# Performance work log

Hardware: AMD Instinct MI355X
Metric: run time of the kernel (lower is better)

Reference implementation:

```python
import jax, jax.numpy as jnp
import numpy as np

N = 100000       # num_nodes
E = 1600000      # num_edges (avg degree 16)
EL = 200000      # link-prediction edges
IN_C = 64
POS = 16
HID = 64
OUT = 32


def setup_inputs() -> dict:
    key = jax.random.key(0)
    ks = jax.random.split(key, 10)
    def glorot(k, shape):
        scale = 1.0 / np.sqrt(shape[0])
        return jax.random.uniform(k, shape, jnp.float32, -scale, scale)
    return {
        "x": jax.random.normal(ks[0], (N, IN_C), jnp.float32),
        "pos_emb": jax.random.normal(ks[1], (N, POS), jnp.float32),
        "W1": glorot(ks[2], (IN_C + POS, HID)),
        "b1": jnp.zeros((HID,), jnp.float32),
        "W2": glorot(ks[3], (HID, OUT)),
        "b2": jnp.zeros((OUT,), jnp.float32),
        "Wl": glorot(ks[4], (2 * OUT, 1)),
        "bl": jnp.zeros((1,), jnp.float32),
        "edge_index": jax.random.randint(ks[5], (2, E), 0, N, jnp.int32),
        "edge_label_index": jax.random.randint(ks[6], (2, EL), 0, N, jnp.int32),
    }


def reference(x, pos_emb, W1, b1, W2, b2, Wl, bl, edge_index, edge_label_index):
    n = x.shape[0]
    # GCNConv: add self-loops, symmetric deg^{-1/2} normalization (PyG defaults)
    loops = jnp.arange(n, dtype=edge_index.dtype)
    src = jnp.concatenate([edge_index[0], loops])  # [E+N]
    dst = jnp.concatenate([edge_index[1], loops])  # [E+N]
    deg = jax.ops.segment_sum(jnp.ones_like(dst, jnp.float32), dst, num_segments=n)
    dinv = jnp.where(deg > 0, jax.lax.rsqrt(jnp.maximum(deg, 1e-12)), 0.0)
    norm = dinv[src] * dinv[dst]  # [E+N]

    def gcn_conv(h, W, b):
        hw = h @ W                                    # [N, d_out] transform first
        msg = hw[src] * norm[:, None]                 # gather + normalize
        return jax.ops.segment_sum(msg, dst, num_segments=n) + b  # scatter-add

    h = jnp.concatenate([x, pos_emb], axis=1)         # [N, in+pos]
    h = jax.nn.relu(gcn_conv(h, W1, b1))              # dropout is eval no-op
    z = gcn_conv(h, W2, b2)                           # [N, out]

    s, d = edge_label_index[0], edge_label_index[1]
    zc = jnp.concatenate([z[s], z[d]], axis=1)        # [EL, 2*out]
    edge_pred = (zc @ Wl + bl)[:, 0]                  # [EL]
    return z, edge_pred
```

## Files before the change

kernel.cpp:

```cpp
#include <hip/hip_runtime.h>
#include <hip/hip_fp16.h>

#define NN 100000
#define NE 1600000
#define NEL 200000

#define NBUCK 196
#define CAPB  10240
#define TPE   8192

typedef short s16x8 __attribute__((ext_vector_type(8)));
typedef float f32x4 __attribute__((ext_vector_type(4)));

__device__ __forceinline__ unsigned short bf16hi(float v) {
    unsigned u = __float_as_uint(v);
    return (unsigned short)((u + 0x7FFFu + ((u >> 16) & 1u)) >> 16);
}
__device__ __forceinline__ float bf16tof(unsigned short b) {
    return __uint_as_float(((unsigned)b) << 16);
}

__global__ __launch_bounds__(256) void k_part(const int* __restrict__ src,
                                              const int* __restrict__ dst,
                                              int* __restrict__ gcur,
                                              int* __restrict__ part) {
    __shared__ int hist[NBUCK];
    __shared__ int base[NBUCK];
    __shared__ int rk[NBUCK];
    int tid = threadIdx.x;
    for (int i = tid; i < NBUCK; i += 256) { hist[i] = 0; rk[i] = 0; }
    __syncthreads();
    int e0 = blockIdx.x * TPE;
    int e1 = min(e0 + TPE, NE);
    for (int e = e0 + tid; e < e1; e += 256)
        atomicAdd(&hist[dst[e] >> 9], 1);
    __syncthreads();
    for (int i = tid; i < NBUCK; i += 256)
        base[i] = i * CAPB + atomicAdd(&gcur[i], hist[i]);
    __syncthreads();
    for (int e = e0 + tid; e < e1; e += 256) {
        int d = dst[e];
        int s = src[e];
        int b = d >> 9;
        int r = atomicAdd(&rk[b], 1);
        part[base[b] + r] = ((d & 511) << 17) | s;
    }
}

__global__ __launch_bounds__(256) void k_build(const int* __restrict__ gcur,
                                               const int* __restrict__ part,
                                               int* __restrict__ csr,
                                               int* __restrict__ off,
                                               float* __restrict__ dinv) {
    __shared__ int cnts[256];
    __shared__ int hist[512];
    __shared__ int loff[512];
    __shared__ int ssum[256];
    __shared__ int csrbuf[CAPB];
    int b = blockIdx.x;
    int tid = threadIdx.x;
    cnts[tid] = (tid < NBUCK) ? gcur[tid] : 0;
    __syncthreads();
    for (int st = 1; st < 256; st <<= 1) {
        int tmp = (tid >= st) ? cnts[tid - st] : 0;
        __syncthreads();
        cnts[tid] += tmp;
        __syncthreads();
    }
    int obase = (b == 0) ? 0 : cnts[b - 1];
    int cnt = gcur[b];
    int pbase = b * CAPB;
    hist[tid] = 0; hist[tid + 256] = 0;
    __syncthreads();
    for (int i = tid; i < cnt; i += 256)
        atomicAdd(&hist[part[pbase + i] >> 17], 1);
    __syncthreads();
    int a0 = hist[2 * tid], a1 = hist[2 * tid + 1];
    int pairs = a0 + a1;
    ssum[tid] = pairs;
    __syncthreads();
    for (int st = 1; st < 256; st <<= 1) {
        int tmp = (tid >= st) ? ssum[tid - st] : 0;
        __syncthreads();
        ssum[tid] += tmp;
        __syncthreads();
    }
    int pexcl = ssum[tid] - pairs;
    loff[2 * tid] = pexcl;
    loff[2 * tid + 1] = pexcl + a0;
    __syncthreads();
    for (int i = tid; i < 512; i += 256) {
        int d = b * 512 + i;
        if (d < NN) {
            int c = hist[i];
            off[d] = obase + loff[i] + c;
            dinv[d] = rsqrtf((float)(c + 1));
        }
    }
    hist[tid] = 0; hist[tid + 256] = 0;
    __syncthreads();
    for (int i = tid; i < cnt; i += 256) {
        int rec = part[pbase + i];
        int dl = rec >> 17;
        int r = atomicAdd(&hist[dl], 1);
        csrbuf[loff[dl] + r] = rec & 0x1FFFF;
    }
    __syncthreads();
    for (int i = tid; i < cnt; i += 256)
        csr[obase + i] = csrbuf[i];
}

#define HW1_K 104
__global__ __launch_bounds__(256) void k_hw1(const float* __restrict__ x,
                                             const float* __restrict__ pos,
                                             const float* __restrict__ W1,
                                             const float* __restrict__ dinv,
                                             __half* __restrict__ hw1) {
    __shared__ unsigned short ahi[64 * HW1_K];
    __shared__ unsigned short alo[64 * HW1_K];
    __shared__ unsigned short bhi[64 * HW1_K];
    __shared__ unsigned short blo[64 * HW1_K];
    __shared__ float sdin[64];
    int tid = threadIdx.x;
    int nb = blockIdx.x * 64;
    for (int i = tid; i < 64 * 24; i += 256) {
        int r = i / 24, c = i - r * 24;
        ahi[r * HW1_K + 80 + c] = 0; alo[r * HW1_K + 80 + c] = 0;
        bhi[r * HW1_K + 80 + c] = 0; blo[r * HW1_K + 80 + c] = 0;
    }
    for (int i = tid; i < 64 * 64; i += 256) {
        int r = i >> 6, c = i & 63;
        int g = nb + r;
        float v = (g < NN) ? x[g * 64 + c] : 0.0f;
        unsigned short h = bf16hi(v);
        ahi[r * HW1_K + c] = h;
        alo[r * HW1_K + c] = bf16hi(v - bf16tof(h));
    }
    for (int i = tid; i < 64 * 16; i += 256) {
        int r = i >> 4, c = i & 15;
        int g = nb + r;
        float v = (g < NN) ? pos[g * 16 + c] : 0.0f;
        unsigned short h = bf16hi(v);
        ahi[r * HW1_K + 64 + c] = h;
        alo[r * HW1_K + 64 + c] = bf16hi(v - bf16tof(h));
    }
    for (int i = tid; i < 80 * 64; i += 256) {
        int k = i >> 6, c = i & 63;
        float v = W1[i];
        unsigned short h = bf16hi(v);
        bhi[c * HW1_K + k] = h;
        blo[c * HW1_K + k] = bf16hi(v - bf16tof(h));
    }
    for (int i = tid; i < 64; i += 256) {
        int g = nb + i;
        sdin[i] = (g < NN) ? dinv[g] : 0.0f;
    }
    __syncthreads();
    int wave = tid >> 6, lane = tid & 63;
    int frow = lane & 15, fq = lane >> 4;
    int r0 = wave * 16;
    int aoff = (r0 + frow) * HW1_K + fq * 8;
    s16x8 ah0 = *(s16x8*)&ahi[aoff];
    s16x8 ah1 = *(s16x8*)&ahi[aoff + 32];
    s16x8 ah2 = *(s16x8*)&ahi[aoff + 64];
    s16x8 al0 = *(s16x8*)&alo[aoff];
    s16x8 al1 = *(s16x8*)&alo[aoff + 32];
    s16x8 al2 = *(s16x8*)&alo[aoff + 64];
    f32x4 acc[4];
#pragma unroll
    for (int ct = 0; ct < 4; ++ct) {
        acc[ct] = (f32x4)(0.0f);
        int boff = (ct * 16 + frow) * HW1_K + fq * 8;
        s16x8 bh0 = *(s16x8*)&bhi[boff];
        s16x8 bh1 = *(s16x8*)&bhi[boff + 32];
        s16x8 bh2 = *(s16x8*)&bhi[boff + 64];
        s16x8 bl0 = *(s16x8*)&blo[boff];
        s16x8 bl1 = *(s16x8*)&blo[boff + 32];
        s16x8 bl2 = *(s16x8*)&blo[boff + 64];
        acc[ct] = __builtin_amdgcn_mfma_f32_16x16x32_bf16(ah0, bh0, acc[ct], 0, 0, 0);
        acc[ct] = __builtin_amdgcn_mfma_f32_16x16x32_bf16(ah1, bh1, acc[ct], 0, 0, 0);
        acc[ct] = __builtin_amdgcn_mfma_f32_16x16x32_bf16(ah2, bh2, acc[ct], 0, 0, 0);
        acc[ct] = __builtin_amdgcn_mfma_f32_16x16x32_bf16(ah0, bl0, acc[ct], 0, 0, 0);
        acc[ct] = __builtin_amdgcn_mfma_f32_16x16x32_bf16(ah1, bl1, acc[ct], 0, 0, 0);
        acc[ct] = __builtin_amdgcn_mfma_f32_16x16x32_bf16(ah2, bl2, acc[ct], 0, 0, 0);
        acc[ct] = __builtin_amdgcn_mfma_f32_16x16x32_bf16(al0, bh0, acc[ct], 0, 0, 0);
        acc[ct] = __builtin_amdgcn_mfma_f32_16x16x32_bf16(al1, bh1, acc[ct], 0, 0, 0);
        acc[ct] = __builtin_amdgcn_mfma_f32_16x16x32_bf16(al2, bh2, acc[ct], 0, 0, 0);
    }
#pragma unroll
    for (int ct = 0; ct < 4; ++ct) {
        int col = ct * 16 + frow;
#pragma unroll
        for (int i = 0; i < 4; ++i) {
            int r = r0 + fq * 4 + i;
            int g = nb + r;
            if (g < NN)
                hw1[g * 64 + col] = __float2half_rn(acc[ct][i] * sdin[r]);
        }
    }
}

__global__ __launch_bounds__(256) void k_gather1(const int* __restrict__ off,
                                                 const int* __restrict__ csr,
                                                 const float* __restrict__ dinv,
                                                 const __half* __restrict__ hw,
                                                 const float* __restrict__ b1,
                                                 __half* __restrict__ h2out) {
    int lane = threadIdx.x & 63;
    int wave = threadIdx.x >> 6;
    int d = blockIdx.x * 4 + wave;
    int start = (d == 0) ? 0 : off[d - 1];
    int end = off[d];
    start = __builtin_amdgcn_readfirstlane(start);
    end   = __builtin_amdgcn_readfirstlane(end);
    float dd = dinv[d];
    float hself = __half2float(hw[d * 64 + lane]);
    float acc0 = 0.0f, acc1 = 0.0f, acc2 = 0.0f, acc3 = 0.0f;
    for (int e = start; e < end; e += 16) {
        int rem = end - e;
        int s0 = csr[e];
        int s1  = (rem > 1)  ? csr[e + 1]  : s0;
        int s2  = (rem > 2)  ? csr[e + 2]  : s0;
        int s3  = (rem > 3)  ? csr[e + 3]  : s0;
        int s4  = (rem > 4)  ? csr[e + 4]  : s0;
        int s5  = (rem > 5)  ? csr[e + 5]  : s0;
        int s6  = (rem > 6)  ? csr[e + 6]  : s0;
        int s7  = (rem > 7)  ? csr[e + 7]  : s0;
        int s8  = (rem > 8)  ? csr[e + 8]  : s0;
        int s9  = (rem > 9)  ? csr[e + 9]  : s0;
        int s10 = (rem > 10) ? csr[e + 10] : s0;
        int s11 = (rem > 11) ? csr[e + 11] : s0;
        int s12 = (rem > 12) ? csr[e + 12] : s0;
        int s13 = (rem > 13) ? csr[e + 13] : s0;
        int s14 = (rem > 14) ? csr[e + 14] : s0;
        int s15 = (rem > 15) ? csr[e + 15] : s0;
        float g0  = __half2float(hw[s0  * 64 + lane]);
        float g1  = __half2float(hw[s1  * 64 + lane]);
        float g2  = __half2float(hw[s2  * 64 + lane]);
        float g3  = __half2float(hw[s3  * 64 + lane]);
        float g4  = __half2float(hw[s4  * 64 + lane]);
        float g5  = __half2float(hw[s5  * 64 + lane]);
        float g6  = __half2float(hw[s6  * 64 + lane]);
        float g7  = __half2float(hw[s7  * 64 + lane]);
        float g8  = __half2float(hw[s8  * 64 + lane]);
        float g9  = __half2float(hw[s9  * 64 + lane]);
        float g10 = __half2float(hw[s10 * 64 + lane]);
        float g11 = __half2float(hw[s11 * 64 + lane]);
        float g12 = __half2float(hw[s12 * 64 + lane]);
        float g13 = __half2float(hw[s13 * 64 + lane]);
        float g14 = __half2float(hw[s14 * 64 + lane]);
        float g15 = __half2float(hw[s15 * 64 + lane]);
        int inv = 16 - rem;
        if (inv < 0) inv = 0;
        acc0 += g0;  acc1 += g1;  acc2 += g2;  acc3 += g3;
        acc0 += g4;  acc1 += g5;  acc2 += g6;  acc3 += g7;
        acc0 += g8;  acc1 += g9;  acc2 += g10; acc3 += g11;
        acc0 += g12; acc1 += g13; acc2 += g14; acc3 += g15;
        acc3 = fmaf(-(float)inv, g0, acc3);
    }
    float v = fmaxf(b1[lane] + dd * (((acc0 + acc1) + (acc2 + acc3)) + hself), 0.0f);
    h2out[d * 64 + lane] = __float2half_rn(v);
}

#define HW2_K 72
__global__ __launch_bounds__(256) void k_hw2(const __half* __restrict__ h2,
                                             const float* __restrict__ W2,
                                             const float* __restrict__ dinv,
                                             __half* __restrict__ hw2) {
    __shared__ unsigned short ahi[128 * HW2_K];
    __shared__ unsigned short alo[128 * HW2_K];
    __shared__ unsigned short bhi[32 * HW2_K];
    __shared__ unsigned short blo[32 * HW2_K];
    __shared__ float sdin[128];
    int tid = threadIdx.x;
    int nb = blockIdx.x * 128;
    for (int i = tid; i < 128 * 32; i += 256) {
        int r = i >> 5, cp = i & 31;
        int g = nb + r;
        __half2 hv = (g < NN) ? ((const __half2*)h2)[g * 32 + cp]
                              : __floats2half2_rn(0.0f, 0.0f);
        float2 f = __half22float2(hv);
        unsigned short h0 = bf16hi(f.x), h1 = bf16hi(f.y);
        ahi[r * HW2_K + 2 * cp]     = h0;
        ahi[r * HW2_K + 2 * cp + 1] = h1;
        alo[r * HW2_K + 2 * cp]     = bf16hi(f.x - bf16tof(h0));
        alo[r * HW2_K + 2 * cp + 1] = bf16hi(f.y - bf16tof(h1));
    }
    for (int i = tid; i < 64 * 32; i += 256) {
        int k = i >> 5, c = i & 31;
        float v = W2[i];
        unsigned short h = bf16hi(v);
        bhi[c * HW2_K + k] = h;
        blo[c * HW2_K + k] = bf16hi(v - bf16tof(h));
    }
    for (int i = tid; i < 128; i += 256) {
        int g = nb + i;
        sdin[i] = (g < NN) ? dinv[g] : 0.0f;
    }
    __syncthreads();
    int wave = tid >> 6, lane = tid & 63;
    int frow = lane & 15, fq = lane >> 4;
    int r0 = wave * 32;
    f32x4 acc[2][2];
#pragma unroll
    for (int rt = 0; rt < 2; ++rt) {
        int aoff = (r0 + rt * 16 + frow) * HW2_K + fq * 8;
        s16x8 ah0 = *(s16x8*)&ahi[aoff];
        s16x8 ah1 = *(s16x8*)&ahi[aoff + 32];
        s16x8 al0 = *(s16x8*)&alo[aoff];
        s16x8 al1 = *(s16x8*)&alo[aoff + 32];
#pragma unroll
        for (int ct = 0; ct < 2; ++ct) {
            acc[rt][ct] = (f32x4)(0.0f);
            int boff = (ct * 16 + frow) * HW2_K + fq * 8;
            s16x8 bh0 = *(s16x8*)&bhi[boff];
            s16x8 bh1 = *(s16x8*)&bhi[boff + 32];
            s16x8 bl0 = *(s16x8*)&blo[boff];
            s16x8 bl1 = *(s16x8*)&blo[boff + 32];
            acc[rt][ct] = __builtin_amdgcn_mfma_f32_16x16x32_bf16(ah0, bh0, acc[rt][ct], 0, 0, 0);
            acc[rt][ct] = __builtin_amdgcn_mfma_f32_16x16x32_bf16(ah1, bh1, acc[rt][ct], 0, 0, 0);
            acc[rt][ct] = __builtin_amdgcn_mfma_f32_16x16x32_bf16(ah0, bl0, acc[rt][ct], 0, 0, 0);
            acc[rt][ct] = __builtin_amdgcn_mfma_f32_16x16x32_bf16(ah1, bl1, acc[rt][ct], 0, 0, 0);
            acc[rt][ct] = __builtin_amdgcn_mfma_f32_16x16x32_bf16(al0, bh0, acc[rt][ct], 0, 0, 0);
            acc[rt][ct] = __builtin_amdgcn_mfma_f32_16x16x32_bf16(al1, bh1, acc[rt][ct], 0, 0, 0);
        }
    }
#pragma unroll
    for (int rt = 0; rt < 2; ++rt)
#pragma unroll
        for (int ct = 0; ct < 2; ++ct) {
            int col = ct * 16 + frow;
#pragma unroll
            for (int i = 0; i < 4; ++i) {
                int r = r0 + rt * 16 + fq * 4 + i;
                int g = nb + r;
                if (g < NN)
                    hw2[g * 32 + col] = __float2half_rn(acc[rt][ct][i] * sdin[r]);
            }
        }
}

__global__ __launch_bounds__(256) void k_gather2(const int* __restrict__ off,
                                                 const int* __restrict__ csr,
                                                 const float* __restrict__ dinv,
                                                 const __half* __restrict__ hw,
                                                 const float* __restrict__ b2,
                                                 const float* __restrict__ Wl,
                                                 float* __restrict__ outz,
                                                 float* __restrict__ uu,
                                                 float* __restrict__ vv) {
    int lane = threadIdx.x & 63;
    int half = lane >> 5;
    int j = lane & 31;
    int wave = threadIdx.x >> 6;
    int d = blockIdx.x * 4 + wave;
    int start = (d == 0) ? 0 : off[d - 1];
    int end = off[d];
    start = __builtin_amdgcn_readfirstlane(start);
    end   = __builtin_amdgcn_readfirstlane(end);
    float dd = dinv[d];
    float hself = __half2float(hw[d * 32 + j]);
    float accA = 0.0f, accB = 0.0f, accC = 0.0f, accD = 0.0f;
    for (int e = start; e < end; e += 16) {
        int rem = end - e;
        int s0 = csr[e];
        int i1 = e + half;
        int sA = (half      < rem) ? csr[i1]      : s0;
        int sB = (half + 2  < rem) ? csr[i1 + 2]  : s0;
        int sC = (half + 4  < rem) ? csr[i1 + 4]  : s0;
        int sD = (half + 6  < rem) ? csr[i1 + 6]  : s0;
        int sE = (half + 8  < rem) ? csr[i1 + 8]  : s0;
        int sF = (half + 10 < rem) ? csr[i1 + 10] : s0;
        int sG = (half + 12 < rem) ? csr[i1 + 12] : s0;
        int sH = (half + 14 < rem) ? csr[i1 + 14] : s0;
        float gA = __half2float(hw[sA * 32 + j]);
        float gB = __half2float(hw[sB * 32 + j]);
        float gC = __half2float(hw[sC * 32 + j]);
        float gD = __half2float(hw[sD * 32 + j]);
        float gE = __half2float(hw[sE * 32 + j]);
        float gF = __half2float(hw[sF * 32 + j]);
        float gG = __half2float(hw[sG * 32 + j]);
        float gH = __half2float(hw[sH * 32 + j]);
        int nv = (rem - half + 1) >> 1;
        if (nv > 8) nv = 8;
        int inv = 8 - nv;
        accA += gA; accB += gB; accC += gC; accD += gD;
        accA += gE; accB += gF; accC += gG; accD += gH;
        accD = fmaf(-(float)inv, gH, accD);
    }
    float acc = (accA + accB) + (accC + accD);
    acc += __shfl(acc, lane ^ 32, 64);
    float z = b2[j] + dd * (acc + hself);
    if (half == 0)
        outz[d * 32 + j] = z;
    float p0 = z * Wl[j];
    float p1 = z * Wl[32 + j];
    p0 += __shfl_xor(p0, 1, 64);  p1 += __shfl_xor(p1, 1, 64);
    p0 += __shfl_xor(p0, 2, 64);  p1 += __shfl_xor(p1, 2, 64);
    p0 += __shfl_xor(p0, 4, 64);  p1 += __shfl_xor(p1, 4, 64);
    p0 += __shfl_xor(p0, 8, 64);  p1 += __shfl_xor(p1, 8, 64);
    p0 += __shfl_xor(p0, 16, 64); p1 += __shfl_xor(p1, 16, 64);
    if (lane == 0) { uu[d] = p0; vv[d] = p1; }
}

__global__ __launch_bounds__(256) void k_linkpred(const int* __restrict__ sidx,
                                                  const int* __restrict__ didx,
                                                  const float* __restrict__ uu,
                                                  const float* __restrict__ vv,
                                                  const float* __restrict__ bl,
                                                  float* __restrict__ pred) {
    int e = blockIdx.x * 256 + threadIdx.x;
    if (e < NEL)
        pred[e] = uu[sidx[e]] + vv[didx[e]] + bl[0];
}

extern "C" void kernel_launch(void* const* d_in, const int* in_sizes, int n_in,
                              void* d_out, int out_size, void* d_ws, size_t ws_size,
                              hipStream_t stream) {
    const float* x    = (const float*)d_in[0];
    const float* pos  = (const float*)d_in[1];
    const float* W1   = (const float*)d_in[2];
    const float* b1   = (const float*)d_in[3];
    const float* W2   = (const float*)d_in[4];
    const float* b2   = (const float*)d_in[5];
    const float* Wl   = (const float*)d_in[6];
    const float* bl   = (const float*)d_in[7];
    const int*   ei   = (const int*)d_in[8];
    const int*   eli  = (const int*)d_in[9];
    const int* src  = ei;
    const int* dst  = ei + NE;
    const int* lsrc = eli;
    const int* ldst = eli + NEL;

    float* out_z    = (float*)d_out;
    float* out_pred = (float*)d_out + NN * 32;

    float*  dinv  = (float*)d_ws;
    int*    off   = (int*)(dinv + NN);
    int*    gcur  = off + NN;
    int*    csr   = gcur + NBUCK;
    __half* hw1   = (__half*)(csr + NE);
    int*    part  = (int*)hw1;
    __half* h2    = hw1 + NN * 64;
    __half* hw2   = h2 + NN * 64;
    float*  uu    = (float*)h2;
    float*  vv    = uu + NN;

    hipMemsetAsync(gcur, 0, NBUCK * sizeof(int), stream);
    k_part<<<(NE + TPE - 1) / TPE, 256, 0, stream>>>(src, dst, gcur, part);
    k_build<<<NBUCK, 256, 0, stream>>>(gcur, part, csr, off, dinv);

    k_hw1<<<(NN + 63) / 64, 256, 0, stream>>>(x, pos, W1, dinv, hw1);

    k_gather1<<<NN / 4, 256, 0, stream>>>(off, csr, dinv, hw1, b1, h2);

    k_hw2<<<(NN + 127) / 128, 256, 0, stream>>>(h2, W2, dinv, hw2);

    k_gather2<<<NN / 4, 256, 0, stream>>>(off, csr, dinv, hw2, b2, Wl,
                                          out_z, uu, vv);

    k_linkpred<<<(NEL + 255) / 256, 256, 0, stream>>>(lsrc, ldst, uu, vv, bl,
                                                      out_pred);
}
```

Baseline: 290.1 us.

## Fuse layer-2 feature transform into layer-1 gather kernel

Removes the separate k_hw2 MFMA kernel and the fp16 h2 intermediate buffer. Each wave in k_gather1 now stages its ReLU output row in shared memory and computes the 64x32 product with W2 using scalar FMAs against a shared copy of W2, writing hw2 directly. This saves a kernel launch and a full N x 64 write and read round trip through memory. In exchange every block reloads W2 into LDS (8 KB per 4 nodes) and the matmul runs on scalar FMA units rather than matrix cores.

```diff
diff --git a/kernel.cpp b/kernel.cpp
--- a/kernel.cpp
+++ b/kernel.cpp
@@ -4,6 +4,7 @@
 #define NN 100000
 #define NE 1600000
 #define NEL 200000
+#define TM 64
 
 #define NBUCK 196
 #define CAPB  10240
@@ -205,9 +206,14 @@
                                                  const float* __restrict__ dinv,
                                                  const __half* __restrict__ hw,
                                                  const float* __restrict__ b1,
-                                                 __half* __restrict__ h2out) {
-    int lane = threadIdx.x & 63;
-    int wave = threadIdx.x >> 6;
+                                                 const float* __restrict__ W2,
+                                                 __half* __restrict__ hw2out) {
+    __shared__ float sW2[64 * 32];
+    __shared__ float h2row[4][64];
+    int tid = threadIdx.x;
+    for (int t = tid; t < 64 * 32; t += 256) sW2[t] = W2[t];
+    int lane = tid & 63;
+    int wave = tid >> 6;
     int d = blockIdx.x * 4 + wave;
     int start = (d == 0) ? 0 : off[d - 1];
     int end = off[d];
@@ -215,6 +221,7 @@
     end   = __builtin_amdgcn_readfirstlane(end);
     float dd = dinv[d];
     float hself = __half2float(hw[d * 64 + lane]);
+    __syncthreads();
     float acc0 = 0.0f, acc1 = 0.0f, acc2 = 0.0f, acc3 = 0.0f;
     for (int e = start; e < end; e += 16) {
         int rem = end - e;
@@ -259,85 +266,18 @@
         acc3 = fmaf(-(float)inv, g0, acc3);
     }
     float v = fmaxf(b1[lane] + dd * (((acc0 + acc1) + (acc2 + acc3)) + hself), 0.0f);
-    h2out[d * 64 + lane] = __float2half_rn(v);
-}
-
-#define HW2_K 72
-__global__ __launch_bounds__(256) void k_hw2(const __half* __restrict__ h2,
-                                             const float* __restrict__ W2,
-                                             const float* __restrict__ dinv,
-                                             __half* __restrict__ hw2) {
-    __shared__ unsigned short ahi[128 * HW2_K];
-    __shared__ unsigned short alo[128 * HW2_K];
-    __shared__ unsigned short bhi[32 * HW2_K];
-    __shared__ unsigned short blo[32 * HW2_K];
-    __shared__ float sdin[128];
-    int tid = threadIdx.x;
-    int nb = blockIdx.x * 128;
-    for (int i = tid; i < 128 * 32; i += 256) {
-        int r = i >> 5, cp = i & 31;
-        int g = nb + r;
-        __half2 hv = (g < NN) ? ((const __half2*)h2)[g * 32 + cp]
-                              : __floats2half2_rn(0.0f, 0.0f);
-        float2 f = __half22float2(hv);
-        unsigned short h0 = bf16hi(f.x), h1 = bf16hi(f.y);
-        ahi[r * HW2_K + 2 * cp]     = h0;
-        ahi[r * HW2_K + 2 * cp + 1] = h1;
-        alo[r * HW2_K + 2 * cp]     = bf16hi(f.x - bf16tof(h0));
-        alo[r * HW2_K + 2 * cp + 1] = bf16hi(f.y - bf16tof(h1));
-    }
-    for (int i = tid; i < 64 * 32; i += 256) {
-        int k = i >> 5, c = i & 31;
-        float v = W2[i];
-        unsigned short h = bf16hi(v);
-        bhi[c * HW2_K + k] = h;
-        blo[c * HW2_K + k] = bf16hi(v - bf16tof(h));
-    }
-    for (int i = tid; i < 128; i += 256) {
-        int g = nb + i;
-        sdin[i] = (g < NN) ? dinv[g] : 0.0f;
-    }
-    __syncthreads();
-    int wave = tid >> 6, lane = tid & 63;
-    int frow = lane & 15, fq = lane >> 4;
-    int r0 = wave * 32;
-    f32x4 acc[2][2];
+    h2row[wave][lane] = v;
+    int j = lane & 31;
+    int half = lane >> 5;
+    float sum = 0.0f;
 #pragma unroll
-    for (int rt = 0; rt < 2; ++rt) {
-        int aoff = (r0 + rt * 16 + frow) * HW2_K + fq * 8;
-        s16x8 ah0 = *(s16x8*)&ahi[aoff];
-        s16x8 ah1 = *(s16x8*)&ahi[aoff + 32];
-        s16x8 al0 = *(s16x8*)&alo[aoff];
-        s16x8 al1 = *(s16x8*)&alo[aoff + 32];
-#pragma unroll
-        for (int ct = 0; ct < 2; ++ct) {
-            acc[rt][ct] = (f32x4)(0.0f);
-            int boff = (ct * 16 + frow) * HW2_K + fq * 8;
-            s16x8 bh0 = *(s16x8*)&bhi[boff];
-            s16x8 bh1 = *(s16x8*)&bhi[boff + 32];
-            s16x8 bl0 = *(s16x8*)&blo[boff];
-            s16x8 bl1 = *(s16x8*)&blo[boff + 32];
-            acc[rt][ct] = __builtin_amdgcn_mfma_f32_16x16x32_bf16(ah0, bh0, acc[rt][ct], 0, 0, 0);
-            acc[rt][ct] = __builtin_amdgcn_mfma_f32_16x16x32_bf16(ah1, bh1, acc[rt][ct], 0, 0, 0);
-            acc[rt][ct] = __builtin_amdgcn_mfma_f32_16x16x32_bf16(ah0, bl0, acc[rt][ct], 0, 0, 0);
-            acc[rt][ct] = __builtin_amdgcn_mfma_f32_16x16x32_bf16(ah1, bl1, acc[rt][ct], 0, 0, 0);
-            acc[rt][ct] = __builtin_amdgcn_mfma_f32_16x16x32_bf16(al0, bh0, acc[rt][ct], 0, 0, 0);
-            acc[rt][ct] = __builtin_amdgcn_mfma_f32_16x16x32_bf16(al1, bh1, acc[rt][ct], 0, 0, 0);
-        }
-    }
-#pragma unroll
-    for (int rt = 0; rt < 2; ++rt)
-#pragma unroll
-        for (int ct = 0; ct < 2; ++ct) {
-            int col = ct * 16 + frow;
-#pragma unroll
-            for (int i = 0; i < 4; ++i) {
-                int r = r0 + rt * 16 + fq * 4 + i;
-                int g = nb + r;
-                if (g < NN)
-                    hw2[g * 32 + col] = __float2half_rn(acc[rt][ct][i] * sdin[r]);
-            }
-        }
+    for (int k = 0; k < 32; ++k) {
+        int kk = half * 32 + k;
+        sum += h2row[wave][kk] * sW2[kk * 32 + j];
+    }
+    sum += __shfl_xor(sum, 32, 64);
+    if (half == 0)
+        hw2out[d * 32 + j] = __float2half_rn(sum * dd);
 }
 
 __global__ __launch_bounds__(256) void k_gather2(const int* __restrict__ off,
@@ -441,20 +381,17 @@
     int*    csr   = gcur + NBUCK;
     __half* hw1   = (__half*)(csr + NE);
     int*    part  = (int*)hw1;
-    __half* h2    = hw1 + NN * 64;
-    __half* hw2   = h2 + NN * 64;
-    float*  uu    = (float*)h2;
+    __half* hw2   = hw1 + NN * 64;
+    float*  uu    = (float*)(hw2 + NN * 32);
     float*  vv    = uu + NN;
 
     hipMemsetAsync(gcur, 0, NBUCK * sizeof(int), stream);
     k_part<<<(NE + TPE - 1) / TPE, 256, 0, stream>>>(src, dst, gcur, part);
     k_build<<<NBUCK, 256, 0, stream>>>(gcur, part, csr, off, dinv);
 
-    k_hw1<<<(NN + 63) / 64, 256, 0, stream>>>(x, pos, W1, dinv, hw1);
-
-    k_gather1<<<NN / 4, 256, 0, stream>>>(off, csr, dinv, hw1, b1, h2);
-
-    k_hw2<<<(NN + 127) / 128, 256, 0, stream>>>(h2, W2, dinv, hw2);
+    k_hw1<<<(NN + TM - 1) / TM, 256, 0, stream>>>(x, pos, W1, dinv, hw1);
+
+    k_gather1<<<NN / 4, 256, 0, stream>>>(off, csr, dinv, hw1, b1, W2, hw2);
 
     k_gather2<<<NN / 4, 256, 0, stream>>>(off, csr, dinv, hw2, b2, Wl,
                                           out_z, uu, vv);
```

Result: faster. 280.2 us (-3.4%).
